# Kernel optimization log

Hardware: AMD Instinct MI355X
Metric: run time of the kernel (lower is better)

## Reference

```python
import jax, jax.numpy as jnp
import numpy as np

STRIDE = 4
NSAMPLE = 16


def setup_inputs() -> dict:
    key = jax.random.key(0)
    k1, k2, k3, k4 = jax.random.split(key, 4)
    N, C, OUT = 16384, 64, 128
    xyz = jax.random.normal(k1, (N, 3), jnp.float32)
    feat = jax.random.normal(k2, (N, C), jnp.float32)
    velocities = jax.random.normal(k3, (N, 3), jnp.float32)
    offset = jnp.array([N // 2, N], dtype=jnp.int32)  # 2 equal ragged segments
    W = jax.random.normal(k4, (OUT, C), jnp.float32) * 0.05  # nn.Linear(64,128,bias=False).weight
    return {"xyz": xyz, "feat": feat, "offset": offset, "velocities": velocities, "W": W}


def _fps(p, m):
    # Farthest point sampling over one segment; first pick is index 0 (pointops convention).
    n = p.shape[0]

    def step(carry, _):
        dists, last = carry
        d = jnp.sum((p - p[last]) ** 2, axis=-1)
        dists = jnp.minimum(dists, d)
        nxt = jnp.argmax(dists).astype(jnp.int32)
        return (dists, nxt), nxt

    dists0 = jnp.full((n,), 1e10, dtype=p.dtype)
    _, rest = jax.lax.scan(step, (dists0, jnp.int32(0)), None, length=m - 1)
    return jnp.concatenate([jnp.zeros((1,), jnp.int32), rest])  # [m]


def reference(xyz, feat, offset, velocities, W):
    B = offset.shape[0]
    N = xyz.shape[0]
    n = N // B          # equal segment size
    m = n // STRIDE     # sampled points per segment
    xyz_b = xyz.reshape(B, n, 3)
    feat_b = feat.reshape(B, n, -1)
    vel_b = velocities.reshape(B, n, -1)
    # FPS in the concatenated xyz|feat space, as in the original (xyzv)
    xyzv_b = jnp.concatenate([xyz_b, feat_b], axis=-1)
    idx = jax.vmap(lambda p: _fps(p, m))(xyzv_b)  # [B, m] int32
    new_xyz_b = jnp.take_along_axis(xyz_b, idx[:, :, None], axis=1)  # [B, m, 3]
    new_vel_b = jnp.take_along_axis(vel_b, idx[:, :, None], axis=1)  # [B, m, 3]
    # kNN query (queryandgroup with feature_only=True): nsample nearest in xyz space
    d2 = (jnp.sum(new_xyz_b ** 2, -1)[:, :, None]
          + jnp.sum(xyz_b ** 2, -1)[:, None, :]
          - 2.0 * jnp.einsum('bmd,bnd->bmn', new_xyz_b, xyz_b))  # [B, m, n]
    _, knn = jax.lax.top_k(-d2, NSAMPLE)  # [B, m, NSAMPLE]
    grouped = jax.vmap(lambda f, i: f[i])(feat_b, knn)  # [B, m, NSAMPLE, C]
    # linear (no bias) -> ReLU -> max-pool over neighbors
    proj = jnp.einsum('bmkc,oc->bmko', grouped, W)
    new_feat = jnp.max(jax.nn.relu(proj), axis=2).reshape(B * m, -1)  # [B*m, OUT]
    # new_offset = cumulative (segment_size // stride)
    counts = jnp.diff(offset, prepend=0) // STRIDE
    new_offset = jnp.cumsum(counts).astype(offset.dtype)
    return (new_xyz_b.reshape(B * m, 3), new_feat, new_offset, new_vel_b.reshape(B * m, -1))
```

## Files before the change

### kernel.cpp

```cpp
#include <hip/hip_runtime.h>
#include <hip/hip_fp16.h>

typedef unsigned long long u64;
typedef __attribute__((ext_vector_type(8))) short bf16x8;
typedef __attribute__((ext_vector_type(4))) float f32x4;

#define SEG_N     8192
#define NSEG      2
#define M_PER_SEG 2048
#define M_TOTAL   4096
#define CFEAT     64
#define COUT      128
#define NSAMPLE   16

#define FPS_WGS_PER_SEG 16
#define FPS_THREADS     512
#define FPS_WAVES       8
#define SLOT_STRIDE     16

#define OUT_XYZ   0
#define OUT_FEAT  12288
#define OUT_OFF   536576
#define OUT_VEL   536578

#define WS_CAND 0
#define WS_FPS  512
#define WS_KNN  16896
#define WS_SQ   (1<<19)
#define WS_D2   (1<<20)
#define D2_SEG8 ((size_t)SEG_N * SEG_N)

#define AG  __HIP_MEMORY_SCOPE_AGENT
#define RLX __ATOMIC_RELAXED

#define REP16(M) M(0) M(1) M(2) M(3) M(4) M(5) M(6) M(7) \
                 M(8) M(9) M(10) M(11) M(12) M(13) M(14) M(15)
#define REP16_EO(E,O) E(0) O(1) E(2) O(3) E(4) O(5) E(6) O(7) \
                      E(8) O(9) E(10) O(11) E(12) O(13) E(14) O(15)

__device__ __forceinline__ unsigned pk2(float a, float b) {
  __half2 h = __floats2half2_rn(a, b);
  unsigned u; __builtin_memcpy(&u, &h, 4); return u;
}
__device__ __forceinline__ float2 up2(unsigned u) {
  __half2 h; __builtin_memcpy(&h, &u, 4);
  return __half22float2(h);
}

template<int CTRL, int RM>
__device__ __forceinline__ unsigned dppmax(unsigned c) {
  int t = __builtin_amdgcn_update_dpp(0, (int)c, CTRL, RM, 0xF, true);
  unsigned u = (unsigned)t;
  return c > u ? c : u;
}

__device__ __forceinline__ short f2bf(float v) {
  return (short)((__float_as_uint(v) + 0x8000u) >> 16);
}


__global__ __launch_bounds__(256)
void norm_kernel(const float* __restrict__ xyz, const float* __restrict__ feat,
                 float* __restrict__ sq)
{
  int i = blockIdx.x * 256 + threadIdx.x;
  if (i >= NSEG * SEG_N) return;
  float a0 = xyz[(size_t)i*3+0], a1 = xyz[(size_t)i*3+1], a2 = xyz[(size_t)i*3+2];
  float acc = a0*a0 + a1*a1 + a2*a2;
  const float4* fr = (const float4*)(feat + (size_t)i * CFEAT);
  #pragma unroll
  for (int k = 0; k < 16; ++k) {
    float4 v = fr[k];
    acc += v.x*v.x + v.y*v.y + v.z*v.z + v.w*v.w;
  }
  sq[i] = acc;
}

#define GKS 104
__global__ __launch_bounds__(256)
void gram_mfma_kernel(const float* __restrict__ xyz, const float* __restrict__ feat,
                      const float* __restrict__ sq, unsigned char* __restrict__ d2m)
{
  __shared__ __align__(16) short Xq[128][GKS];
  __shared__ __align__(16) short Xp[128][GKS];
  __shared__ float sqs[128], sps[128];

  const int b   = blockIdx.x;
  const int s   = b >> 12;
  const int rem = b & 4095;
  const int tq  = rem >> 6;
  const int tp  = rem & 63;
  const int q0  = tq * 128, p0 = tp * 128;
  const int tid = threadIdx.x;
  unsigned char* d2seg = d2m + (size_t)s * D2_SEG8;

  for (int e = tid; e < 128 * 96; e += 256) {
    int r = e / 96, c = e - r * 96;
    size_t gq = (size_t)(s * SEG_N + q0 + r);
    size_t gp = (size_t)(s * SEG_N + p0 + r);
    float vq = 0.f, vp = 0.f;
    if (c < 3)        { vq = xyz[gq*3 + c];          vp = xyz[gp*3 + c]; }
    else if (c < 67)  { vq = feat[gq*CFEAT + (c-3)]; vp = feat[gp*CFEAT + (c-3)]; }
    Xq[r][c] = f2bf(vq);
    Xp[r][c] = f2bf(vp);
  }
  if (tid < 128)      sqs[tid] = sq[s * SEG_N + q0 + tid];
  else                sps[tid - 128] = sq[s * SEG_N + p0 + (tid - 128)];
  __syncthreads();

  const int lane = tid & 63;
  const int wv   = tid >> 6;
  const int wr   = wv >> 1, wc = wv & 1;
  const int lrow = lane & 15;
  const int kgr  = (lane >> 4) * 8;

  f32x4 acc[4][4];
  #pragma unroll
  for (int i = 0; i < 4; ++i)
    #pragma unroll
    for (int j = 0; j < 4; ++j) acc[i][j] = (f32x4){0.f,0.f,0.f,0.f};

  #pragma unroll
  for (int ch = 0; ch < 3; ++ch) {
    bf16x8 af[4], bf[4];
    #pragma unroll
    for (int i = 0; i < 4; ++i)
      af[i] = *(const bf16x8*)&Xq[wr*64 + i*16 + lrow][ch*32 + kgr];
    #pragma unroll
    for (int j = 0; j < 4; ++j)
      bf[j] = *(const bf16x8*)&Xp[wc*64 + j*16 + lrow][ch*32 + kgr];
    #pragma unroll
    for (int i = 0; i < 4; ++i)
      #pragma unroll
      for (int j = 0; j < 4; ++j)
        acc[i][j] = __builtin_amdgcn_mfma_f32_16x16x32_bf16(af[i], bf[j],
                                                            acc[i][j], 0, 0, 0);
  }
  __syncthreads();

  unsigned char* ob = (unsigned char*)&Xq[0][0];
  #pragma unroll
  for (int i = 0; i < 4; ++i) {
    #pragma unroll
    for (int j = 0; j < 4; ++j) {
      #pragma unroll
      for (int reg = 0; reg < 4; ++reg) {
        int r  = wr*64 + i*16 + (lane >> 4)*4 + reg;
        int cl = wc*64 + j*16 + (lane & 15);
        float d2 = sqs[r] + sps[cl] - 2.f * acc[i][j][reg];
        unsigned o;
        if (q0 + r == p0 + cl) o = 0u;
        else {
          d2 = fmaxf(d2, 0.f);
          o = __float2uint_rn(fminf(d2, 255.f));
        }
        ob[(r << 7) + cl] = (unsigned char)o;
      }
    }
  }
  __syncthreads();

  const unsigned* obu = (const unsigned*)ob;
  for (int e = tid; e < 4096; e += 256) {
    int r = e >> 5, cw = e & 31;
    *(unsigned*)&d2seg[((size_t)(q0 + r) << 13) + p0 + cw*4] = obu[e];
  }
}

__global__ __launch_bounds__(1024)
void fps_fast8_kernel(const unsigned char* __restrict__ d2m,
                      int* __restrict__ fps_idx)
{
  __shared__ unsigned wslot[2][16];

  const int tid  = threadIdx.x;
  const int lane = tid & 63;
  const int wv   = tid >> 6;
  const int s    = blockIdx.x;
  const int p0   = tid * 8;
  const unsigned idx0 = 8191 - p0;
  const unsigned char* base_s = d2m + (size_t)s * D2_SEG8;

  unsigned D0=255u,D1=255u,D2v=255u,D3=255u,D4=255u,D5=255u,D6=255u,D7=255u;

  if (tid == 0) fps_idx[s * M_PER_SEG] = 0;
  int q = 0;

  for (int t = 1; t < M_PER_SEG; ++t) {
    uint2 w = *(const uint2*)(base_s + ((size_t)q << 13) + p0);
    unsigned a = w.x, b = w.y;
    D0 = min(D0,  a        & 255u);
    D1 = min(D1, (a >>  8) & 255u);
    D2v= min(D2v,(a >> 16) & 255u);
    D3 = min(D3,  a >> 24);
    D4 = min(D4,  b        & 255u);
    D5 = min(D5, (b >>  8) & 255u);
    D6 = min(D6, (b >> 16) & 255u);
    D7 = min(D7,  b >> 24);

    unsigned c = (D0 << 13) | idx0;
    c = max(c, (D1 << 13) | (idx0 - 1u));
    c = max(c, (D2v<< 13) | (idx0 - 2u));
    c = max(c, (D3 << 13) | (idx0 - 3u));
    c = max(c, (D4 << 13) | (idx0 - 4u));
    c = max(c, (D5 << 13) | (idx0 - 5u));
    c = max(c, (D6 << 13) | (idx0 - 6u));
    c = max(c, (D7 << 13) | (idx0 - 7u));

    c = dppmax<0x111, 0xF>(c);
    c = dppmax<0x112, 0xF>(c);
    c = dppmax<0x114, 0xF>(c);
    c = dppmax<0x118, 0xF>(c);
    c = dppmax<0x142, 0xA>(c);
    c = dppmax<0x143, 0xC>(c);
    unsigned wmax = (unsigned)__builtin_amdgcn_readlane((int)c, 63);

    if (lane == 0) wslot[t & 1][wv] = wmax;
    __syncthreads();

    unsigned v = wslot[t & 1][lane & 15];
    v = dppmax<0x111, 0xF>(v);
    v = dppmax<0x112, 0xF>(v);
    v = dppmax<0x114, 0xF>(v);
    v = dppmax<0x118, 0xF>(v);
    unsigned gmax = (unsigned)__builtin_amdgcn_readlane((int)v, 15);
    q = 8191 - (int)(gmax & 0x1FFFu);
    if (tid == 0) fps_idx[s * M_PER_SEG + t] = q;
  }
}

__global__ __attribute__((amdgpu_waves_per_eu(2, 2)))
__launch_bounds__(FPS_THREADS)
void fps_kernel(const float* __restrict__ xyz, const float* __restrict__ feat,
                u64* __restrict__ cand, int* __restrict__ fps_idx)
{
#pragma clang fp contract(off)
  __shared__ u64 wslot[FPS_WAVES];
  __shared__ int qidx_sh;

  const int tid  = threadIdx.x;
  const int lane = tid & 63;
  const int wv   = tid >> 6;
  const int s    = blockIdx.x >> 4;
  const int wg   = blockIdx.x & 15;
  const int pl   = wg * FPS_THREADS + tid;
  const size_t gr = (size_t)(s * SEG_N + pl);

  float px, py, pz;
#define DECLP(k) uint2 pp##k;
  REP16(DECLP)
  px = xyz[gr*3+0]; py = xyz[gr*3+1]; pz = xyz[gr*3+2];
  {
    const float4* fr = (const float4*)(feat + gr * CFEAT);
#define LOADP(k) { float4 v = fr[k]; pp##k.x = pk2(v.x, v.y); pp##k.y = pk2(v.z, v.w); }
    REP16(LOADP)
  }

  float qx, qy, qz;
#define DECLQ(k) float4 qf##k;
  REP16(DECLQ)
#define LOADQ1(k) qf##k = frq[k];
#define LOAD_Q(qb) { \
    qx = xyz[(qb)*3+0]; qy = xyz[(qb)*3+1]; qz = xyz[(qb)*3+2]; \
    const float4* frq = (const float4*)(feat + (qb) * CFEAT); \
    REP16(LOADQ1) }

  LOAD_Q((size_t)(s * SEG_N))
  if (tid == 0 && wg == 0) fps_idx[s * M_PER_SEG] = 0;

  float D = 1e10f;

  for (int t = 1; t < M_PER_SEG; ++t) {
    float r0=0.f, r1=0.f, r2=0.f, r3=0.f, r4=0.f, r5=0.f, r6=0.f, r7=0.f;
    {
      float tt;
      tt = px - qx; r0 += tt*tt;
      tt = py - qy; r1 += tt*tt;
      tt = pz - qz; r2 += tt*tt;
    }
#define DE(k) { float2 ab = up2(pp##k.x), cd = up2(pp##k.y); \
                float t0 = ab.x - qf##k.x; r3 += t0*t0; \
                float t1 = ab.y - qf##k.y; r4 += t1*t1; \
                float t2 = cd.x - qf##k.z; r5 += t2*t2; \
                float t3 = cd.y - qf##k.w; r6 += t3*t3; }
#define DO(k) { float2 ab = up2(pp##k.x), cd = up2(pp##k.y); \
                float t0 = ab.x - qf##k.x; r7 += t0*t0; \
                float t1 = ab.y - qf##k.y; r0 += t1*t1; \
                float t2 = cd.x - qf##k.z; r1 += t2*t2; \
                float t3 = cd.y - qf##k.w; r2 += t3*t3; }
    REP16_EO(DE, DO)
    float a = ((r0+r1)+(r2+r3)) + ((r4+r5)+(r6+r7));
    D = fminf(D, a);

    float bd = D; int bi = pl;
    #pragma unroll
    for (int off = 32; off >= 1; off >>= 1) {
      float od = __shfl_xor(bd, off);
      int   oi = __shfl_xor(bi, off);
      if (od > bd || (od == bd && oi < bi)) { bd = od; bi = oi; }
    }
    if (lane == 0)
      wslot[wv] = ((u64)__float_as_uint(bd) << 13) | (u64)(unsigned)(8191 - bi);
    __syncthreads();

    if (wv == 0) {
      u64 w = (lane < FPS_WAVES) ? wslot[lane] : 0ULL;
      #pragma unroll
      for (int off = 4; off >= 1; off >>= 1) {
        u64 o = __shfl_xor(w, off, 8);
        if (o > w) w = o;
      }
      u64* base = &cand[(((unsigned)t & 1u) * NSEG + s) * SLOT_STRIDE];
      if (lane == 0)
        __hip_atomic_store(&base[wg], ((u64)(unsigned)t << 45) | w, RLX, AG);

      u64 v = 0;
      if (lane < FPS_WGS_PER_SEG) {
        v = __hip_atomic_load(&base[lane], RLX, AG);
        while ((unsigned)(v >> 45) != (unsigned)t) {
          __builtin_amdgcn_s_sleep(1);
          v = __hip_atomic_load(&base[lane], RLX, AG);
        }
      }
      #pragma unroll
      for (int off = 8; off >= 1; off >>= 1) {
        u64 o = __shfl_xor(v, off, 16);
        if (o > v) v = o;
      }
      int qi = 8191 - (int)(v & 0x1FFFu);
      if (lane == 0) {
        qidx_sh = qi;
        if (wg == 0) fps_idx[s * M_PER_SEG + t] = qi;
      }
    }
    __syncthreads();

    LOAD_Q((size_t)(s * SEG_N + qidx_sh))
  }
}

__global__ void gather_kernel(const float* __restrict__ xyz, const float* __restrict__ vel,
                              const int* __restrict__ fps_idx, float* __restrict__ out)
{
  int i = blockIdx.x * 256 + threadIdx.x;
  if (i >= M_TOTAL) return;
  int s = i >> 11, r = i & 2047;
  int g = s * SEG_N + (fps_idx[s * M_PER_SEG + r] & 8191);
  out[OUT_XYZ + i*3 + 0] = xyz[(size_t)g*3 + 0];
  out[OUT_XYZ + i*3 + 1] = xyz[(size_t)g*3 + 1];
  out[OUT_XYZ + i*3 + 2] = xyz[(size_t)g*3 + 2];
  out[OUT_VEL + i*3 + 0] = vel[(size_t)g*3 + 0];
  out[OUT_VEL + i*3 + 1] = vel[(size_t)g*3 + 1];
  out[OUT_VEL + i*3 + 2] = vel[(size_t)g*3 + 2];
  if (i == 0) { out[OUT_OFF] = 2048.0f; out[OUT_OFF + 1] = 4096.0f; }
}

#define KNN_TILE 1024
__global__ __launch_bounds__(256)
void knn_kernel(const float* __restrict__ xyz, const float* __restrict__ out,
                int* __restrict__ knn)
{
  __shared__ float px[KNN_TILE], py[KNN_TILE], pz[KNN_TILE];
  __shared__ float ldK[16][16][16];
  __shared__ float Tq[16];
  __shared__ float dbuf[16][24];
  __shared__ int   cbuf[16][24];
  __shared__ int   cnt[16];

  const int tid = threadIdx.x;
  const int ql = tid >> 4, j = tid & 15;
  const int qg = blockIdx.x * 16 + ql;
  const int s  = qg >> 11;
  const float qx = out[OUT_XYZ + qg*3 + 0];
  const float qy = out[OUT_XYZ + qg*3 + 1];
  const float qz = out[OUT_XYZ + qg*3 + 2];
  const float sq = qx*qx + qy*qy + qz*qz;

  float K[16];
  #pragma unroll
  for (int r = 0; r < 16; ++r) K[r] = 3.4e38f;

  for (int tile = 0; tile < SEG_N / KNN_TILE; ++tile) {
    __syncthreads();
    for (int u = tid; u < KNN_TILE; u += 256) {
      size_t g = (size_t)(s * SEG_N + tile * KNN_TILE + u);
      px[u] = xyz[g*3+0]; py[u] = xyz[g*3+1]; pz[u] = xyz[g*3+2];
    }
    __syncthreads();
    #pragma unroll 4
    for (int i = 0; i < KNN_TILE / 16; ++i) {
      int c = i * 16 + j;
      float x = px[c], y = py[c], z = pz[c];
      float sp  = x*x + y*y + z*z;
      float dot = qx*x + qy*y + qz*z;
      float d2  = (sq + sp) - 2.0f * dot;
      #pragma unroll
      for (int r = 15; r >= 1; --r)
        K[r] = fminf(fmaxf(d2, K[r-1]), K[r]);
      K[0] = fminf(K[0], d2);
    }
  }
  #pragma unroll
  for (int r = 0; r < 16; ++r) ldK[ql][j][r] = K[r];
  __syncthreads();

  {
    int head = 0;
    float T = 3.4e38f;
    for (int r = 0; r < 16; ++r) {
      float val = (head < 16) ? ldK[ql][j][head] : 3.4e38f;
      float mv = val; int ml = j;
      #pragma unroll
      for (int off = 8; off >= 1; off >>= 1) {
        float ov = __shfl_xor(mv, off, 16);
        int   ol = __shfl_xor(ml, off, 16);
        if (ov < mv || (ov == mv && ol < ml)) { mv = ov; ml = ol; }
      }
      if (j == ml) head++;
      T = mv;
    }
    if (j == 0) { Tq[ql] = T; cnt[ql] = 0; }
  }
  __syncthreads();
  const float T  = Tq[ql];
  const float Tm = T + fabsf(T) * 1e-6f + 1e-30f;

  for (int tile = 0; tile < SEG_N / KNN_TILE; ++tile) {
    __syncthreads();
    for (int u = tid; u < KNN_TILE; u += 256) {
      size_t g = (size_t)(s * SEG_N + tile * KNN_TILE + u);
      px[u] = xyz[g*3+0]; py[u] = xyz[g*3+1]; pz[u] = xyz[g*3+2];
    }
    __syncthreads();
    for (int i = 0; i < KNN_TILE / 16; ++i) {
      int c = i * 16 + j;
      float x = px[c], y = py[c], z = pz[c];
      float sp  = x*x + y*y + z*z;
      float dot = qx*x + qy*y + qz*z;
      float d2  = (sq + sp) - 2.0f * dot;
      if (d2 <= Tm) {
        int pos = atomicAdd(&cnt[ql], 1);
        if (pos < 24) { dbuf[ql][pos] = d2; cbuf[ql][pos] = tile * KNN_TILE + c; }
      }
    }
  }
  __syncthreads();

  if (j == 0) {
    int n = cnt[ql]; if (n > 24) n = 24;
    for (int r = 0; r < NSAMPLE; ++r) {
      float bv = 3.4e38f; int bc = 0, bp = -1;
      for (int e = 0; e < n; ++e) {
        float dv = dbuf[ql][e]; int cc = cbuf[ql][e];
        if (dv < bv || (dv == bv && cc < bc)) { bv = dv; bc = cc; bp = e; }
      }
      if (bp >= 0) dbuf[ql][bp] = 3.4e38f;
      knn[qg * NSAMPLE + r] = bc;
    }
  }
}

__global__ __launch_bounds__(128)
void gemm_kernel(const float* __restrict__ feat, const float* __restrict__ W,
                 const int* __restrict__ knn, float* __restrict__ out)
{
  __shared__ __align__(16) float f[NSAMPLE][CFEAT];
  __shared__ int kid[NSAMPLE];
  const int tid = threadIdx.x;
  const int q = blockIdx.x;
  const int s = q >> 11;
  if (tid < NSAMPLE) kid[tid] = knn[q * NSAMPLE + tid] & 8191;
  __syncthreads();
  for (int e = tid; e < NSAMPLE * CFEAT; e += 128) {
    int k = e >> 6, c = e & 63;
    f[k][c] = feat[(size_t)(s * SEG_N + kid[k]) * CFEAT + c];
  }
  float4 w[16];
  const float4* Wrow = (const float4*)(W + (size_t)tid * CFEAT);
  #pragma unroll
  for (int c4 = 0; c4 < 16; ++c4) w[c4] = Wrow[c4];
  __syncthreads();

  float m = -3.4e38f;
  #pragma unroll
  for (int k = 0; k < NSAMPLE; ++k) {
    float acc = 0.f;
    const float4* frow = (const float4*)&f[k][0];
    #pragma unroll
    for (int c4 = 0; c4 < 16; ++c4) {
      float4 fv = frow[c4];
      acc += fv.x * w[c4].x + fv.y * w[c4].y + fv.z * w[c4].z + fv.w * w[c4].w;
    }
    m = fmaxf(m, acc);
  }
  out[OUT_FEAT + (size_t)q * COUT + tid] = fmaxf(m, 0.f);
}

extern "C" void kernel_launch(void* const* d_in, const int* in_sizes, int n_in,
                              void* d_out, int out_size, void* d_ws, size_t ws_size,
                              hipStream_t stream)
{
  const float* xyz  = (const float*)d_in[0];
  const float* feat = (const float*)d_in[1];
  const float* vel  = (const float*)d_in[3];
  const float* W    = (const float*)d_in[4];
  float* out = (float*)d_out;
  char*  ws  = (char*)d_ws;
  u64* cand    = (u64*)(ws + WS_CAND);
  int* fps_idx = (int*)(ws + WS_FPS);
  int* knn     = (int*)(ws + WS_KNN);

  if (ws_size >= (size_t)WS_D2 + NSEG * D2_SEG8) {
    float* sq = (float*)(ws + WS_SQ);
    unsigned char* d2m = (unsigned char*)(ws + WS_D2);
    norm_kernel<<<(NSEG * SEG_N) / 256, 256, 0, stream>>>(xyz, feat, sq);
    gram_mfma_kernel<<<NSEG * 64 * 64, 256, 0, stream>>>(xyz, feat, sq, d2m);
    fps_fast8_kernel<<<NSEG, 1024, 0, stream>>>(d2m, fps_idx);
  } else {
    hipMemsetAsync(cand, 0, 512, stream);
    fps_kernel<<<NSEG * FPS_WGS_PER_SEG, FPS_THREADS, 0, stream>>>(
        xyz, feat, cand, fps_idx);
  }
  gather_kernel<<<M_TOTAL / 256, 256, 0, stream>>>(xyz, vel, fps_idx, out);
  knn_kernel<<<M_TOTAL / 16, 256, 0, stream>>>(xyz, out, knn);
  gemm_kernel<<<M_TOTAL, 128, 0, stream>>>(feat, W, knn, out);
}
```

Measured before the change: 2.100 ms.

## Speculatively prefetch the runner-up FPS row to hide the serial load latency

The FPS loop now also computes the second-best wave maximum each step and prefetches that candidate's distance row. If the next selected index matches the prediction, the prefetched row is used instead of issuing a dependent global load. This is meant to take memory latency off the serial per-iteration critical path, at the cost of an extra reduction and an extra load every step. The prediction only holds when the next pick equals the current runner-up, which may be rare given that distances change after each update.

New measurement: 2.272 ms. 1.08x slower.

```diff
diff --git a/kernel.cpp b/kernel.cpp
--- a/kernel.cpp
+++ b/kernel.cpp
@@ -184,11 +184,13 @@
   unsigned D0=255u,D1=255u,D2v=255u,D3=255u,D4=255u,D5=255u,D6=255u,D7=255u;
 
   if (tid == 0) fps_idx[s * M_PER_SEG] = 0;
-  int q = 0;
+
+  uint2 cur = *(const uint2*)(base_s + p0);
+  uint2 Pf  = cur;
+  int pred = -1;
 
   for (int t = 1; t < M_PER_SEG; ++t) {
-    uint2 w = *(const uint2*)(base_s + ((size_t)q << 13) + p0);
-    unsigned a = w.x, b = w.y;
+    unsigned a = cur.x, b = cur.y;
     D0 = min(D0,  a        & 255u);
     D1 = min(D1, (a >>  8) & 255u);
     D2v= min(D2v,(a >> 16) & 255u);
@@ -219,13 +221,31 @@
     __syncthreads();
 
     unsigned v = wslot[t & 1][lane & 15];
-    v = dppmax<0x111, 0xF>(v);
-    v = dppmax<0x112, 0xF>(v);
-    v = dppmax<0x114, 0xF>(v);
-    v = dppmax<0x118, 0xF>(v);
-    unsigned gmax = (unsigned)__builtin_amdgcn_readlane((int)v, 15);
-    q = 8191 - (int)(gmax & 0x1FFFu);
+    unsigned m = v;
+    m = dppmax<0x111, 0xF>(m);
+    m = dppmax<0x112, 0xF>(m);
+    m = dppmax<0x114, 0xF>(m);
+    m = dppmax<0x118, 0xF>(m);
+    unsigned gmax = (unsigned)__builtin_amdgcn_readlane((int)m, 15);
+
+    unsigned v2 = (v == gmax) ? 0u : v;
+    v2 = dppmax<0x111, 0xF>(v2);
+    v2 = dppmax<0x112, 0xF>(v2);
+    v2 = dppmax<0x114, 0xF>(v2);
+    v2 = dppmax<0x118, 0xF>(v2);
+    unsigned g2 = (unsigned)__builtin_amdgcn_readlane((int)v2, 15);
+
+    int q  = 8191 - (int)(gmax & 0x1FFFu);
+    int rn = 8191 - (int)(g2 & 0x1FFFu);
     if (tid == 0) fps_idx[s * M_PER_SEG + t] = q;
+
+    if (q == pred) {
+      cur = Pf;
+    } else {
+      cur = *(const uint2*)(base_s + ((size_t)q << 13) + p0);
+    }
+    Pf   = *(const uint2*)(base_s + ((size_t)rn << 13) + p0);
+    pred = rn;
   }
 }
 
```
